# Kernel tuning notes

Hardware: AMD Instinct MI355X
Metric: run time of the kernel (lower is better)

Reference implementation:

```python
import jax, jax.numpy as jnp
import numpy as np

# ---- constants matching init_kwargs ----
NUM_STEPS = 25
NEW_AMP = 2.0
ENC_THRESHOLD = 0.5   # encoder spike threshold
BETA = 0.95           # LIF leak
LIF_THRESHOLD = 1.0   # snntorch Leaky default threshold
FIL_LEN = 50
FIL_STD = 5.0


def _gaussian_window(M, std):
    n = np.arange(M, dtype=np.float32) - (M - 1) / 2.0
    return np.exp(-0.5 * (n / std) ** 2).astype(np.float32)


def setup_inputs() -> dict:
    key = jax.random.key(0)
    k1, k2, k3 = jax.random.split(key, 3)
    B, L, H, C = 131072, 187, 50, 5
    x = jax.random.normal(k1, (B, L), dtype=jnp.float32)
    filt = jnp.asarray(_gaussian_window(FIL_LEN, FIL_STD))
    W1 = jax.random.normal(k2, (H, L), dtype=jnp.float32) / np.sqrt(L)
    W2 = jax.random.normal(k3, (C, H), dtype=jnp.float32) / np.sqrt(H)
    return {"x": x, "filt": filt, "W1": W1, "W2": W2}


def _encoder(x, filt):
    # Gaussian smoothing (conv1d, SAME padding), amplify, threshold -> spikes
    B, L = x.shape
    K = filt.shape[0]
    y = jax.lax.conv_general_dilated(
        x[:, None, :], filt[None, None, :],
        window_strides=(1,), padding=[((K - 1) // 2, K // 2)],
        dimension_numbers=("NCH", "OIH", "NCH"))[:, 0, :]
    y = y * NEW_AMP
    return (y > ENC_THRESHOLD).astype(x.dtype)


def reference(x, filt, W1, W2):
    spikes = _encoder(x, filt)                 # [B, L], identical every step
    cur1 = spikes @ W1.T                       # [B, 50], constant over steps
    B = x.shape[0]
    mem1 = jnp.zeros((B, W1.shape[0]), x.dtype)
    mem2 = jnp.zeros((B, W2.shape[0]), x.dtype)

    def step(carry, _):
        m1, m2 = carry
        m1 = BETA * m1 + cur1
        spk1 = (m1 > LIF_THRESHOLD).astype(m1.dtype)
        m1 = m1 - spk1 * LIF_THRESHOLD         # reset-by-subtraction
        cur2 = spk1 @ W2.T
        m2 = BETA * m2 + cur2
        spk2 = (m2 > LIF_THRESHOLD).astype(m2.dtype)
        m2 = m2 - spk2 * LIF_THRESHOLD
        return (m1, m2), spk2

    (_, _), spk_rec = jax.lax.scan(step, (mem1, mem2), None, length=NUM_STEPS)
    spike_count = spikes.sum() * NUM_STEPS     # encoder.count_spike()
    return spk_rec, spike_count
```

## Files before the change

kernel.cpp:

```cpp
#include <hip/hip_runtime.h>


typedef float    f32x4 __attribute__((ext_vector_type(4)));
typedef float    f32x2 __attribute__((ext_vector_type(2)));
typedef short    s16x8 __attribute__((ext_vector_type(8)));

constexpr int L = 187;
constexpr int H = 50;
constexpr int NST = 25;
constexpr float BETA = 0.95f;
constexpr float YTH  = 0.25f;

constexpr int FT_STR = 264;
constexpr int FT_SH  = 8 * FT_STR;
constexpr int W1A_SH = 4 * 6 * 64 * 8;
constexpr int W2A_SH = 2 * 64 * 8;
constexpr int NPART  = 4096;

__device__ inline unsigned short f2bf(float f) {
    union { float f; unsigned u; } v; v.f = f;
    return (unsigned short)((v.u + 0x7FFFu + ((v.u >> 16) & 1u)) >> 16);
}

__global__ void __launch_bounds__(256) prep_frags(
    const float* __restrict__ filt, const float* __restrict__ W1,
    const float* __restrict__ W2, unsigned short* __restrict__ frags)
{
    int i = blockIdx.x * 256 + threadIdx.x;
    if (i < FT_SH) {
        int r = i / FT_STR, m = i - r * FT_STR;
        int idx = m + r - 48;
        frags[i] = (idx >= 0 && idx < 50) ? f2bf(filt[idx]) : (unsigned short)0;
    } else if (i < FT_SH + W1A_SH) {
        int i2 = i - FT_SH;
        int jj = i2 & 7, lane = (i2 >> 3) & 63, kt = (i2 >> 9) % 6, mt = i2 / (512 * 6);
        int lm = lane & 15, lk = lane >> 4;
        int h = 16 * mt + lm;
        int l = 4 * lk + (jj & 3) + 16 * (2 * kt + (jj >> 2));
        unsigned short v = 0;
        if (h < H && l < L) v = f2bf(W1[h * L + l]);
        frags[i] = v;
    } else if (i < FT_SH + W1A_SH + W2A_SH) {
        int i3 = i - FT_SH - W1A_SH;
        int jj = i3 & 7, lane = (i3 >> 3) & 63, kt = i3 >> 9;
        int lm = lane & 15, lk = lane >> 4;
        int h = 4 * lk + (jj & 3) + 16 * (2 * kt + (jj >> 2));
        unsigned short v = 0;
        if (lm < 5 && h < H) v = f2bf(W2[lm * H + h]);
        frags[i] = v;
    }
}

__global__ void __launch_bounds__(256, 4) snn_fused(
    const float* __restrict__ x,
    const unsigned short* __restrict__ frags,
    float* __restrict__ out, unsigned int* __restrict__ part, int B)
{
    __shared__ __align__(16) unsigned short ftabL[FT_SH];
    __shared__ __align__(16) unsigned short W1L[W1A_SH];
    __shared__ __align__(16) unsigned short W2L[W2A_SH];
    __shared__ unsigned int csh[4];

    const int tid = threadIdx.x;
    const int wid = tid >> 6, lane = tid & 63;
    const int lm = lane & 15, lk = lane >> 4;
    const int row = blockIdx.x * 64 + wid * 16 + lm;

    {
        const uint4* g = (const uint4*)frags;
        uint4* sF = (uint4*)ftabL;
        uint4* s1 = (uint4*)W1L;
        uint4* s2 = (uint4*)W2L;
        #pragma unroll 2
        for (int i = tid; i < 264; i += 256) sF[i] = g[i];
        #pragma unroll
        for (int i = tid; i < 1536; i += 256) s1[i] = g[264 + i];
        if (tid < 128) s2[tid] = g[264 + 1536 + tid];
    }
    __syncthreads();

    s16x8 xB[6];
    {
        const float* __restrict__ xr = x + (size_t)row * L;
        #pragma unroll
        for (int kt = 0; kt < 6; ++kt) {
            const int k0 = 32 * kt + 8 * lk;
            s16x8 v;
            if (k0 + 8 <= L) {
                float t[8];
                __builtin_memcpy(t, xr + k0, 32);
                #pragma unroll
                for (int jj = 0; jj < 8; ++jj) v[jj] = (short)f2bf(t[jj]);
            } else {
                #pragma unroll
                for (int jj = 0; jj < 8; ++jj) {
                    int k = k0 + jj;
                    v[jj] = (short)f2bf((k < L) ? xr[k] : 0.f);
                }
            }
            xB[kt] = v;
        }
    }

    const int dl = 8 * lk - lm + 72;
    unsigned int scnt = 0;
    s16x8 spkB[6];
    {
        constexpr int lo[6] = {0, 0, 1, 2, 3, 4};
        constexpr int hi[6] = {1, 2, 3, 4, 5, 5};
        #pragma unroll
        for (int p = 0; p < 6; ++p) {
            f32x4 y0 = (f32x4){0, 0, 0, 0}, y1 = (f32x4){0, 0, 0, 0};
            #pragma unroll
            for (int kt = 0; kt < 6; ++kt) {
                if (kt >= lo[p] && kt <= hi[p]) {
                    const int D0a = dl + 32 * kt - 32 * p;
                    const int D0b = D0a - 16;
                    s16x8 a0 = *(const s16x8*)&ftabL[(D0a & 7) * FT_STR + (D0a & ~7)];
                    s16x8 a1 = *(const s16x8*)&ftabL[(D0b & 7) * FT_STR + (D0b & ~7)];
                    y0 = __builtin_amdgcn_mfma_f32_16x16x32_bf16(a0, xB[kt], y0, 0, 0, 0);
                    y1 = __builtin_amdgcn_mfma_f32_16x16x32_bf16(a1, xB[kt], y1, 0, 0, 0);
                }
            }
            union { unsigned w[4]; s16x8 v; } pk;
            #pragma unroll
            for (int w = 0; w < 4; ++w) {
                float va = (w < 2) ? y0[2 * w]     : y1[2 * (w - 2)];
                float vb = (w < 2) ? y0[2 * w + 1] : y1[2 * (w - 2) + 1];
                bool s0 = va > YTH, s1 = vb > YTH;
                bool c0 = s0, c1 = s1;
                if (p == 5 && w >= 2) {
                    c0 = s0 && ((4 * lk + 2 * (w - 2))     < 11);
                    c1 = s1 && ((4 * lk + 2 * (w - 2) + 1) < 11);
                }
                scnt += (unsigned)__popcll(__ballot(c0));
                scnt += (unsigned)__popcll(__ballot(c1));
                pk.w[w] = (s0 ? 0x3F80u : 0u) | (s1 ? 0x3F800000u : 0u);
            }
            spkB[p] = pk.v;
        }
    }
    if (lane == 0) csh[wid] = scnt;
    __syncthreads();
    if (tid == 0) part[blockIdx.x] = csh[0] + csh[1] + csh[2] + csh[3];

    f32x4 cu[4];
    #pragma unroll
    for (int mt = 0; mt < 4; ++mt) cu[mt] = (f32x4){0, 0, 0, 0};
    #pragma unroll
    for (int mt = 0; mt < 4; ++mt)
        #pragma unroll
        for (int kt = 0; kt < 6; ++kt) {
            s16x8 a = *(const s16x8*)&W1L[((mt * 6 + kt) * 64 + lane) * 8];
            cu[mt] = __builtin_amdgcn_mfma_f32_16x16x32_bf16(a, spkB[kt], cu[mt], 0, 0, 0);
        }

    s16x8 w2a[2];
    #pragma unroll
    for (int kt = 0; kt < 2; ++kt)
        w2a[kt] = *(const s16x8*)&W2L[(kt * 64 + lane) * 8];

    f32x2 cup[4][2], m1p[4][2];
    #pragma unroll
    for (int mt = 0; mt < 4; ++mt) {
        cup[mt][0] = (f32x2){cu[mt][0], cu[mt][1]};
        cup[mt][1] = (f32x2){cu[mt][2], cu[mt][3]};
        m1p[mt][0] = (f32x2){0.f, 0.f};
        m1p[mt][1] = (f32x2){0.f, 0.f};
    }
    f32x4 m2 = (f32x4){0, 0, 0, 0};
    const f32x2 B2 = (f32x2){BETA, BETA};
    const f32x4 B4 = (f32x4){BETA, BETA, BETA, BETA};

    float* __restrict__ po = out + (size_t)row * 5;
    const size_t step = (size_t)B * 5;

    #pragma unroll 5
    for (int t = 0; t < NST; ++t) {
        unsigned pw[8];
        pw[7] = 0u;
        #pragma unroll
        for (int mt = 0; mt < 4; ++mt) {
            #pragma unroll
            for (int hf = 0; hf < 2; ++hf) {
                if (mt == 3 && hf == 1) continue;
                f32x2 m = B2 * m1p[mt][hf] + cup[mt][hf];
                float s0 = (m[0] > 1.f) ? 1.f : 0.f;
                float s1 = (m[1] > 1.f) ? 1.f : 0.f;
                pw[2 * mt + hf] = __builtin_amdgcn_perm(
                    __float_as_uint(s1), __float_as_uint(s0), 0x07060302u);
                m1p[mt][hf] = m - (f32x2){s0, s1};
            }
        }
        union { unsigned w[4]; s16x8 v; } u0, u1;
        u0.w[0] = pw[0]; u0.w[1] = pw[1]; u0.w[2] = pw[2]; u0.w[3] = pw[3];
        u1.w[0] = pw[4]; u1.w[1] = pw[5]; u1.w[2] = pw[6]; u1.w[3] = pw[7];
        f32x4 c2a = (f32x4){0, 0, 0, 0}, c2b = (f32x4){0, 0, 0, 0};
        c2a = __builtin_amdgcn_mfma_f32_16x16x32_bf16(w2a[0], u0.v, c2a, 0, 0, 0);
        c2b = __builtin_amdgcn_mfma_f32_16x16x32_bf16(w2a[1], u1.v, c2b, 0, 0, 0);
        f32x4 mm = B4 * m2 + (c2a + c2b);
        f32x4 sv;
        #pragma unroll
        for (int j = 0; j < 4; ++j) sv[j] = (mm[j] > 1.f) ? 1.f : 0.f;
        m2 = mm - sv;
        float* __restrict__ pt = po + (size_t)t * step;
        if (lk == 0) {
            __builtin_memcpy(pt, &sv, 16);
        } else if (lk == 1) {
            pt[4] = sv[0];
        }
    }
}

__global__ void __launch_bounds__(256) finalize_count(
    const unsigned int* __restrict__ part, int n,
    float* __restrict__ out, size_t off)
{
    __shared__ unsigned int sh[4];
    unsigned int s = 0;
    for (int i = threadIdx.x; i < n; i += 256) s += part[i];
    #pragma unroll
    for (int o = 32; o; o >>= 1) s += __shfl_down(s, o);
    if ((threadIdx.x & 63) == 0) sh[threadIdx.x >> 6] = s;
    __syncthreads();
    if (threadIdx.x == 0) {
        unsigned int t = sh[0] + sh[1] + sh[2] + sh[3];
        out[off] = (float)((double)t * 25.0);
    }
}

__global__ void __launch_bounds__(256) snn_fallback(
    const float* __restrict__ x, const float* __restrict__ filt,
    const float* __restrict__ W1, const float* __restrict__ W2,
    float* __restrict__ out, unsigned int* __restrict__ part, int B)
{
    __shared__ unsigned int csh[4];
    const int row = blockIdx.x * 256 + threadIdx.x;
    const bool valid = row < B;
    const int rr = valid ? row : (B - 1);
    const float* __restrict__ xr = x + (size_t)rr * L;
    float w[64], cur1[H];
    #pragma unroll
    for (int h = 0; h < H; ++h) cur1[h] = 0.f;
    int cntv = 0;
    #pragma unroll
    for (int i = 0; i < 64; ++i) w[i] = (i >= 24) ? xr[i - 24] : 0.f;
    #pragma unroll 1
    for (int s = 0; s < 12; ++s) {
        const int l0 = s * 15;
        #pragma unroll
        for (int j = 0; j < 15; ++j) {
            const int l = l0 + j;
            float yv = 0.f;
            #pragma unroll
            for (int k = 0; k < 50; ++k) yv = fmaf(w[j + k], filt[k], yv);
            const bool sb = yv > YTH;
            cntv += sb;
            const float sp = sb ? 1.f : 0.f;
            #pragma unroll
            for (int h = 0; h < H; ++h) cur1[h] = fmaf(sp, W1[h * L + l], cur1[h]);
        }
        #pragma unroll
        for (int i = 0; i < 49; ++i) w[i] = w[i + 15];
        #pragma unroll
        for (int d = 0; d < 15; ++d) {
            const int g = l0 + 40 + d;
            w[49 + d] = (g < L) ? xr[g] : 0.f;
        }
    }
    #pragma unroll
    for (int j = 0; j < 7; ++j) {
        const int l = 180 + j;
        float yv = 0.f;
        #pragma unroll
        for (int k = 0; k < 50; ++k) yv = fmaf(w[j + k], filt[k], yv);
        const bool sb = yv > YTH;
        cntv += sb;
        const float sp = sb ? 1.f : 0.f;
        #pragma unroll
        for (int h = 0; h < H; ++h) cur1[h] = fmaf(sp, W1[h * L + l], cur1[h]);
    }
    int wc = valid ? cntv : 0;
    #pragma unroll
    for (int off = 32; off; off >>= 1) wc += __shfl_down(wc, off);
    if ((threadIdx.x & 63) == 0) csh[threadIdx.x >> 6] = (unsigned)wc;
    __syncthreads();
    if (threadIdx.x == 0) part[blockIdx.x] = csh[0] + csh[1] + csh[2] + csh[3];
    float m1[H], m2[5];
    #pragma unroll
    for (int h = 0; h < H; ++h) m1[h] = 0.f;
    #pragma unroll
    for (int c = 0; c < 5; ++c) m2[c] = 0.f;
    #pragma unroll 1
    for (int t = 0; t < NST; ++t) {
        float c2[5] = {0, 0, 0, 0, 0};
        #pragma unroll
        for (int h = 0; h < H; ++h) {
            float m = fmaf(BETA, m1[h], cur1[h]);
            const float sp = (m > 1.f) ? 1.f : 0.f;
            m1[h] = m - sp;
            #pragma unroll
            for (int c = 0; c < 5; ++c) c2[c] = fmaf(sp, W2[c * H + h], c2[c]);
        }
        float* __restrict__ ot = out + ((size_t)t * B + rr) * 5;
        #pragma unroll
        for (int c = 0; c < 5; ++c) {
            float m = fmaf(BETA, m2[c], c2[c]);
            const float s2 = (m > 1.f) ? 1.f : 0.f;
            m2[c] = m - s2;
            if (valid) ot[c] = s2;
        }
    }
}

extern "C" void kernel_launch(void* const* d_in, const int* in_sizes, int n_in,
                              void* d_out, int out_size, void* d_ws, size_t ws_size,
                              hipStream_t stream)
{
    const float* x    = (const float*)d_in[0];
    const float* filt = (const float*)d_in[1];
    const float* W1   = (const float*)d_in[2];
    const float* W2   = (const float*)d_in[3];
    float* out        = (float*)d_out;
    const int B       = in_sizes[0] / L;

    unsigned int* part    = (unsigned int*)d_ws;
    unsigned short* frags = (unsigned short*)((char*)d_ws + NPART * 4);
    const int total_sh    = FT_SH + W1A_SH + W2A_SH;
    const size_t need     = (size_t)NPART * 4 + (size_t)total_sh * 2;

    if (ws_size >= need && (B % 64) == 0 && B / 64 <= NPART) {
        prep_frags<<<(total_sh + 255) / 256, 256, 0, stream>>>(filt, W1, W2, frags);
        snn_fused<<<B / 64, 256, 0, stream>>>(x, frags, out, part, B);
        finalize_count<<<1, 256, 0, stream>>>(part, B / 64, out, (size_t)NST * B * 5);
    } else {
        snn_fallback<<<(B + 255) / 256, 256, 0, stream>>>(x, filt, W1, W2, out, part, B);
        finalize_count<<<1, 256, 0, stream>>>(part, (B + 255) / 256, out, (size_t)NST * B * 5);
    }
}
```

Measured before the change: 55.68 us.

## Process two 16-row tiles per wave to reuse filter and weight fragments

Each wave now handles two 16-row tiles instead of one, and the grid is halved to B/128 blocks. Filter fragments loaded from LDS and W1/W2 fragments are shared across both tiles, and the two tiles' MFMA chains interleave to hide latency. The time-step loop runs both tiles per iteration with unroll 1, replacing unroll 5. This roughly doubles live registers, which may lower occupancy under launch_bounds(256,4), and it halves the number of blocks and the cost of loading shared tables per row.

```diff
diff --git a/kernel.cpp b/kernel.cpp
--- a/kernel.cpp
+++ b/kernel.cpp
@@ -64,7 +64,7 @@
     const int tid = threadIdx.x;
     const int wid = tid >> 6, lane = tid & 63;
     const int lm = lane & 15, lk = lane >> 4;
-    const int row = blockIdx.x * 64 + wid * 16 + lm;
+    const int tp = (blockIdx.x * 4 + wid) * 2;
 
     {
         const uint4* g = (const uint4*)frags;
@@ -79,9 +79,10 @@
     }
     __syncthreads();
 
-    s16x8 xB[6];
-    {
-        const float* __restrict__ xr = x + (size_t)row * L;
+    s16x8 xB[2][6];
+    #pragma unroll
+    for (int T = 0; T < 2; ++T) {
+        const float* __restrict__ xr = x + (size_t)((tp + T) * 16 + lm) * L;
         #pragma unroll
         for (int kt = 0; kt < 6; ++kt) {
             const int k0 = 32 * kt + 8 * lk;
@@ -98,19 +99,21 @@
                     v[jj] = (short)f2bf((k < L) ? xr[k] : 0.f);
                 }
             }
-            xB[kt] = v;
+            xB[T][kt] = v;
         }
     }
 
     const int dl = 8 * lk - lm + 72;
     unsigned int scnt = 0;
-    s16x8 spkB[6];
+    s16x8 spkB[2][6];
     {
         constexpr int lo[6] = {0, 0, 1, 2, 3, 4};
         constexpr int hi[6] = {1, 2, 3, 4, 5, 5};
         #pragma unroll
         for (int p = 0; p < 6; ++p) {
-            f32x4 y0 = (f32x4){0, 0, 0, 0}, y1 = (f32x4){0, 0, 0, 0};
+            f32x4 y[2][2];
+            y[0][0] = (f32x4){0,0,0,0}; y[0][1] = (f32x4){0,0,0,0};
+            y[1][0] = (f32x4){0,0,0,0}; y[1][1] = (f32x4){0,0,0,0};
             #pragma unroll
             for (int kt = 0; kt < 6; ++kt) {
                 if (kt >= lo[p] && kt <= hi[p]) {
@@ -118,41 +121,50 @@
                     const int D0b = D0a - 16;
                     s16x8 a0 = *(const s16x8*)&ftabL[(D0a & 7) * FT_STR + (D0a & ~7)];
                     s16x8 a1 = *(const s16x8*)&ftabL[(D0b & 7) * FT_STR + (D0b & ~7)];
-                    y0 = __builtin_amdgcn_mfma_f32_16x16x32_bf16(a0, xB[kt], y0, 0, 0, 0);
-                    y1 = __builtin_amdgcn_mfma_f32_16x16x32_bf16(a1, xB[kt], y1, 0, 0, 0);
+                    y[0][0] = __builtin_amdgcn_mfma_f32_16x16x32_bf16(a0, xB[0][kt], y[0][0], 0, 0, 0);
+                    y[0][1] = __builtin_amdgcn_mfma_f32_16x16x32_bf16(a1, xB[0][kt], y[0][1], 0, 0, 0);
+                    y[1][0] = __builtin_amdgcn_mfma_f32_16x16x32_bf16(a0, xB[1][kt], y[1][0], 0, 0, 0);
+                    y[1][1] = __builtin_amdgcn_mfma_f32_16x16x32_bf16(a1, xB[1][kt], y[1][1], 0, 0, 0);
                 }
             }
-            union { unsigned w[4]; s16x8 v; } pk;
-            #pragma unroll
-            for (int w = 0; w < 4; ++w) {
-                float va = (w < 2) ? y0[2 * w]     : y1[2 * (w - 2)];
-                float vb = (w < 2) ? y0[2 * w + 1] : y1[2 * (w - 2) + 1];
-                bool s0 = va > YTH, s1 = vb > YTH;
-                bool c0 = s0, c1 = s1;
-                if (p == 5 && w >= 2) {
-                    c0 = s0 && ((4 * lk + 2 * (w - 2))     < 11);
-                    c1 = s1 && ((4 * lk + 2 * (w - 2) + 1) < 11);
+            #pragma unroll
+            for (int T = 0; T < 2; ++T) {
+                union { unsigned w[4]; s16x8 v; } pk;
+                #pragma unroll
+                for (int w = 0; w < 4; ++w) {
+                    float va = (w < 2) ? y[T][0][2 * w]     : y[T][1][2 * (w - 2)];
+                    float vb = (w < 2) ? y[T][0][2 * w + 1] : y[T][1][2 * (w - 2) + 1];
+                    bool s0 = va > YTH, s1 = vb > YTH;
+                    bool c0 = s0, c1 = s1;
+                    if (p == 5 && w >= 2) {
+                        c0 = s0 && ((4 * lk + 2 * (w - 2))     < 11);
+                        c1 = s1 && ((4 * lk + 2 * (w - 2) + 1) < 11);
+                    }
+                    scnt += (unsigned)__popcll(__ballot(c0));
+                    scnt += (unsigned)__popcll(__ballot(c1));
+                    pk.w[w] = (s0 ? 0x3F80u : 0u) | (s1 ? 0x3F800000u : 0u);
                 }
-                scnt += (unsigned)__popcll(__ballot(c0));
-                scnt += (unsigned)__popcll(__ballot(c1));
-                pk.w[w] = (s0 ? 0x3F80u : 0u) | (s1 ? 0x3F800000u : 0u);
-            }
-            spkB[p] = pk.v;
+                spkB[T][p] = pk.v;
+            }
         }
     }
     if (lane == 0) csh[wid] = scnt;
     __syncthreads();
     if (tid == 0) part[blockIdx.x] = csh[0] + csh[1] + csh[2] + csh[3];
 
-    f32x4 cu[4];
-    #pragma unroll
-    for (int mt = 0; mt < 4; ++mt) cu[mt] = (f32x4){0, 0, 0, 0};
+    f32x4 cu[2][4];
+    #pragma unroll
+    for (int mt = 0; mt < 4; ++mt) {
+        cu[0][mt] = (f32x4){0, 0, 0, 0};
+        cu[1][mt] = (f32x4){0, 0, 0, 0};
+    }
     #pragma unroll
     for (int mt = 0; mt < 4; ++mt)
         #pragma unroll
         for (int kt = 0; kt < 6; ++kt) {
             s16x8 a = *(const s16x8*)&W1L[((mt * 6 + kt) * 64 + lane) * 8];
-            cu[mt] = __builtin_amdgcn_mfma_f32_16x16x32_bf16(a, spkB[kt], cu[mt], 0, 0, 0);
+            cu[0][mt] = __builtin_amdgcn_mfma_f32_16x16x32_bf16(a, spkB[0][kt], cu[0][mt], 0, 0, 0);
+            cu[1][mt] = __builtin_amdgcn_mfma_f32_16x16x32_bf16(a, spkB[1][kt], cu[1][mt], 0, 0, 0);
         }
 
     s16x8 w2a[2];
@@ -160,54 +172,64 @@
     for (int kt = 0; kt < 2; ++kt)
         w2a[kt] = *(const s16x8*)&W2L[(kt * 64 + lane) * 8];
 
-    f32x2 cup[4][2], m1p[4][2];
-    #pragma unroll
-    for (int mt = 0; mt < 4; ++mt) {
-        cup[mt][0] = (f32x2){cu[mt][0], cu[mt][1]};
-        cup[mt][1] = (f32x2){cu[mt][2], cu[mt][3]};
-        m1p[mt][0] = (f32x2){0.f, 0.f};
-        m1p[mt][1] = (f32x2){0.f, 0.f};
-    }
-    f32x4 m2 = (f32x4){0, 0, 0, 0};
+    f32x2 cup[2][4][2], m1p[2][4][2];
+    #pragma unroll
+    for (int T = 0; T < 2; ++T)
+        #pragma unroll
+        for (int mt = 0; mt < 4; ++mt) {
+            cup[T][mt][0] = (f32x2){cu[T][mt][0], cu[T][mt][1]};
+            cup[T][mt][1] = (f32x2){cu[T][mt][2], cu[T][mt][3]};
+            m1p[T][mt][0] = (f32x2){0.f, 0.f};
+            m1p[T][mt][1] = (f32x2){0.f, 0.f};
+        }
+    f32x4 m2[2];
+    m2[0] = (f32x4){0, 0, 0, 0};
+    m2[1] = (f32x4){0, 0, 0, 0};
     const f32x2 B2 = (f32x2){BETA, BETA};
     const f32x4 B4 = (f32x4){BETA, BETA, BETA, BETA};
 
-    float* __restrict__ po = out + (size_t)row * 5;
+    float* __restrict__ po[2];
+    po[0] = out + (size_t)(tp * 16 + lm) * 5;
+    po[1] = out + (size_t)((tp + 1) * 16 + lm) * 5;
     const size_t step = (size_t)B * 5;
 
-    #pragma unroll 5
+    #pragma unroll 1
     for (int t = 0; t < NST; ++t) {
-        unsigned pw[8];
-        pw[7] = 0u;
-        #pragma unroll
-        for (int mt = 0; mt < 4; ++mt) {
-            #pragma unroll
-            for (int hf = 0; hf < 2; ++hf) {
-                if (mt == 3 && hf == 1) continue;
-                f32x2 m = B2 * m1p[mt][hf] + cup[mt][hf];
-                float s0 = (m[0] > 1.f) ? 1.f : 0.f;
-                float s1 = (m[1] > 1.f) ? 1.f : 0.f;
-                pw[2 * mt + hf] = __builtin_amdgcn_perm(
-                    __float_as_uint(s1), __float_as_uint(s0), 0x07060302u);
-                m1p[mt][hf] = m - (f32x2){s0, s1};
-            }
-        }
-        union { unsigned w[4]; s16x8 v; } u0, u1;
-        u0.w[0] = pw[0]; u0.w[1] = pw[1]; u0.w[2] = pw[2]; u0.w[3] = pw[3];
-        u1.w[0] = pw[4]; u1.w[1] = pw[5]; u1.w[2] = pw[6]; u1.w[3] = pw[7];
-        f32x4 c2a = (f32x4){0, 0, 0, 0}, c2b = (f32x4){0, 0, 0, 0};
-        c2a = __builtin_amdgcn_mfma_f32_16x16x32_bf16(w2a[0], u0.v, c2a, 0, 0, 0);
-        c2b = __builtin_amdgcn_mfma_f32_16x16x32_bf16(w2a[1], u1.v, c2b, 0, 0, 0);
-        f32x4 mm = B4 * m2 + (c2a + c2b);
-        f32x4 sv;
-        #pragma unroll
-        for (int j = 0; j < 4; ++j) sv[j] = (mm[j] > 1.f) ? 1.f : 0.f;
-        m2 = mm - sv;
-        float* __restrict__ pt = po + (size_t)t * step;
-        if (lk == 0) {
-            __builtin_memcpy(pt, &sv, 16);
-        } else if (lk == 1) {
-            pt[4] = sv[0];
+        const size_t toff = (size_t)t * step;
+        #pragma unroll
+        for (int T = 0; T < 2; ++T) {
+            unsigned pw[8];
+            pw[7] = 0u;
+            #pragma unroll
+            for (int mt = 0; mt < 4; ++mt) {
+                #pragma unroll
+                for (int hf = 0; hf < 2; ++hf) {
+                    if (mt == 3 && hf == 1) continue;
+                    f32x2 m = B2 * m1p[T][mt][hf] + cup[T][mt][hf];
+                    float s0 = (m[0] > 1.f) ? 1.f : 0.f;
+                    float s1 = (m[1] > 1.f) ? 1.f : 0.f;
+                    pw[2 * mt + hf] = __builtin_amdgcn_perm(
+                        __float_as_uint(s1), __float_as_uint(s0), 0x07060302u);
+                    m1p[T][mt][hf] = m - (f32x2){s0, s1};
+                }
+            }
+            union { unsigned w[4]; s16x8 v; } u0, u1;
+            u0.w[0] = pw[0]; u0.w[1] = pw[1]; u0.w[2] = pw[2]; u0.w[3] = pw[3];
+            u1.w[0] = pw[4]; u1.w[1] = pw[5]; u1.w[2] = pw[6]; u1.w[3] = pw[7];
+            f32x4 c2a = (f32x4){0, 0, 0, 0}, c2b = (f32x4){0, 0, 0, 0};
+            c2a = __builtin_amdgcn_mfma_f32_16x16x32_bf16(w2a[0], u0.v, c2a, 0, 0, 0);
+            c2b = __builtin_amdgcn_mfma_f32_16x16x32_bf16(w2a[1], u1.v, c2b, 0, 0, 0);
+            f32x4 mm = B4 * m2[T] + (c2a + c2b);
+            f32x4 sv;
+            #pragma unroll
+            for (int j = 0; j < 4; ++j) sv[j] = (mm[j] > 1.f) ? 1.f : 0.f;
+            m2[T] = mm - sv;
+            float* __restrict__ pt = po[T] + toff;
+            if (lk == 0) {
+                __builtin_memcpy(pt, &sv, 16);
+            } else if (lk == 1) {
+                pt[4] = sv[0];
+            }
         }
     }
 }
@@ -329,10 +351,10 @@
     const int total_sh    = FT_SH + W1A_SH + W2A_SH;
     const size_t need     = (size_t)NPART * 4 + (size_t)total_sh * 2;
 
-    if (ws_size >= need && (B % 64) == 0 && B / 64 <= NPART) {
+    if (ws_size >= need && (B % 128) == 0 && B / 128 <= NPART) {
         prep_frags<<<(total_sh + 255) / 256, 256, 0, stream>>>(filt, W1, W2, frags);
-        snn_fused<<<B / 64, 256, 0, stream>>>(x, frags, out, part, B);
-        finalize_count<<<1, 256, 0, stream>>>(part, B / 64, out, (size_t)NST * B * 5);
+        snn_fused<<<B / 128, 256, 0, stream>>>(x, frags, out, part, B);
+        finalize_count<<<1, 256, 0, stream>>>(part, B / 128, out, (size_t)NST * B * 5);
     } else {
         snn_fallback<<<(B + 255) / 256, 256, 0, stream>>>(x, filt, W1, W2, out, part, B);
         finalize_count<<<1, 256, 0, stream>>>(part, (B + 255) / 256, out, (size_t)NST * B * 5);
```

After: 61.15 us. 9.8% more time.
